# Performance work log

Hardware: AMD Instinct MI355X
Metric: run time of the kernel (lower is better)

Reference implementation:

```python
import jax, jax.numpy as jnp
import numpy as np

# NF4 quantization levels (16 entries) from NF4Quantizer
NF4_LEVELS = jnp.array([
    -1.0, -0.6961928009986877, -0.5250730514526367, -0.39491748809814453,
    -0.28444138169288635, -0.18477343022823334, -0.09105003625154495, 0.0,
    0.07958029955625534, 0.16093020141124725, 0.24611230194568634,
    0.33791524171829224, 0.44070982933044434, 0.5626170039176941,
    0.7229568362236023, 1.0], dtype=jnp.float32)

OUT_F, IN_F = 4096, 4096
B, S = 2, 512

def setup_inputs() -> dict:
    key = jax.random.key(0)
    k1, k2, k3, k4, k5 = jax.random.split(key, 5)
    x = jax.random.normal(k1, (B, S, IN_F), dtype=jnp.float32)
    w0 = jax.random.normal(k2, (OUT_F, IN_F), dtype=jnp.float32) * 0.02
    nf4_idx = jax.random.randint(k3, (OUT_F, IN_F), 0, 16, dtype=jnp.int32)
    scale = jax.random.uniform(k4, (1,), dtype=jnp.float32) * 0.1 + 0.01
    zero_point = jax.random.normal(k5, (1,), dtype=jnp.float32) * 0.01
    return {"x": x, "w0": w0, "nf4_idx": nf4_idx, "scale": scale,
            "zero_point": zero_point}

def reference(x, w0, nf4_idx, scale, zero_point):
    # NF4 dequantize: look up level values, then affine (quantized*scale + zp)
    q = NF4_LEVELS[nf4_idx]                      # [out, in] float32
    deq_w = q * scale + zero_point               # dequantized adaptor weight
    # frozen base linear + dequantized low-rank-adaptor linear (QLoRA-style)
    base = jnp.einsum('bsi,oi->bso', x, w0)
    adapt = jnp.einsum('bsi,oi->bso', x, deq_w)
    return base + adapt
```

## Files before the change

### kernel.cpp

```cpp
#include <hip/hip_runtime.h>
#include <hip/hip_bf16.h>
#include <stdint.h>

#define MDIM 1024
#define NDIM 4096
#define KDIM 4096

#define BM 128
#define BN 128
#define BK 64

typedef __attribute__((ext_vector_type(4))) float f32x4;
typedef __attribute__((ext_vector_type(4))) float float4v;
typedef __attribute__((ext_vector_type(4))) int int4v;
typedef __attribute__((ext_vector_type(4))) unsigned int uint4v;
typedef __attribute__((ext_vector_type(8))) short short8;

#define GLOBAL_AS __attribute__((address_space(1)))
#define LDS_AS __attribute__((address_space(3)))

#define HARD_BARRIER() do {                               \
    __builtin_amdgcn_sched_barrier(0);                    \
    asm volatile("s_waitcnt lgkmcnt(0)" ::: "memory");    \
    __builtin_amdgcn_s_barrier();                         \
    asm volatile("" ::: "memory");                        \
    __builtin_amdgcn_sched_barrier(0);                    \
} while (0)

__device__ __constant__ float c_nf4[16] = {
    -1.0f, -0.6961928009986877f, -0.5250730514526367f, -0.39491748809814453f,
    -0.28444138169288635f, -0.18477343022823334f, -0.09105003625154495f, 0.0f,
    0.07958029955625534f, 0.16093020141124725f, 0.24611230194568634f,
    0.33791524171829224f, 0.44070982933044434f, 0.5626170039176941f,
    0.7229568362236023f, 1.0f};

__device__ __forceinline__ unsigned bf16_rne(float f) {
    unsigned u = __float_as_uint(f);
    return (u + 0x7fffu + ((u >> 16) & 1u)) >> 16;
}

#define W_BLOCKS ((NDIM * KDIM) / (256 * 8))
#define X_BLOCKS ((MDIM * KDIM) / (256 * 8))

__global__ __launch_bounds__(256) void prep_kernel(
    const float* __restrict__ x, const float* __restrict__ w0,
    const int* __restrict__ nf4_idx, const float* __restrict__ scale_p,
    const float* __restrict__ zp_p, __hip_bfloat16* __restrict__ Wc,
    __hip_bfloat16* __restrict__ xb)
{
    const int lane = threadIdx.x & 63;
    if (blockIdx.x < W_BLOCKS) {
        const float scale = scale_p[0];
        const float zp = zp_p[0];
        const int tab = __float_as_int(c_nf4[lane & 15] * scale + zp);
        const size_t base = ((size_t)blockIdx.x * 256 + threadIdx.x) * 8;
        int4v i0 = *(const int4v*)(nf4_idx + base);
        int4v i1 = *(const int4v*)(nf4_idx + base + 4);
        float4v w_0 = *(const float4v*)(w0 + base);
        float4v w_1 = *(const float4v*)(w0 + base + 4);
        unsigned r[8];
#pragma unroll
        for (int j = 0; j < 4; j++) {
            float q = __int_as_float(__builtin_amdgcn_ds_bpermute(i0[j] * 4, tab));
            r[j] = bf16_rne(w_0[j] + q);
        }
#pragma unroll
        for (int j = 0; j < 4; j++) {
            float q = __int_as_float(__builtin_amdgcn_ds_bpermute(i1[j] * 4, tab));
            r[4 + j] = bf16_rne(w_1[j] + q);
        }
        uint4v st;
        st.x = r[0] | (r[1] << 16);
        st.y = r[2] | (r[3] << 16);
        st.z = r[4] | (r[5] << 16);
        st.w = r[6] | (r[7] << 16);
        *(uint4v*)((unsigned short*)Wc + base) = st;
    } else {
        const size_t base = ((size_t)(blockIdx.x - W_BLOCKS) * 256 + threadIdx.x) * 8;
        float4v a0 = *(const float4v*)(x + base);
        float4v a1 = *(const float4v*)(x + base + 4);
        uint4v st;
        st.x = bf16_rne(a0[0]) | (bf16_rne(a0[1]) << 16);
        st.y = bf16_rne(a0[2]) | (bf16_rne(a0[3]) << 16);
        st.z = bf16_rne(a1[0]) | (bf16_rne(a1[1]) << 16);
        st.w = bf16_rne(a1[2]) | (bf16_rne(a1[3]) << 16);
        *(uint4v*)((unsigned short*)xb + base) = st;
    }
}

__global__ __launch_bounds__(512) void gemm_kernel(
    const __hip_bfloat16* __restrict__ A,
    const __hip_bfloat16* __restrict__ B,
    float* __restrict__ C)
{
    __shared__ __hip_bfloat16 sm[3][2][BM * BK];

    const int tid = threadIdx.x;
    const int lane = tid & 63;
    const int w = tid >> 6;
    const int wr = w >> 2;
    const int wc = (w >> 1) & 1;
    const int wk = w & 1;

    const int bid = blockIdx.x;
    const int orig = (bid & 7) * 32 + (bid >> 3);
    const int mtile = orig & 7;
    const int ntile = orig >> 3;

    const int s_subrow = lane >> 3;
    const int s_chunkpos = lane & 7;
    int s_row[2], s_goff[2];
#pragma unroll
    for (int j = 0; j < 2; j++) {
        int row = w * 16 + j * 8 + s_subrow;
        s_row[j] = row;
        s_goff[j] = (s_chunkpos ^ (row & 7)) * 8;
    }

#define STAGE(buf, kt) do {                                                        \
    _Pragma("unroll")                                                              \
    for (int j = 0; j < 2; j++) {                                                  \
        const __hip_bfloat16* ga = A + (size_t)(mtile * BM + s_row[j]) * KDIM      \
                                     + (kt) * BK + s_goff[j];                      \
        __builtin_amdgcn_global_load_lds((const GLOBAL_AS void*)ga,                \
            (LDS_AS void*)&sm[buf][0][(w * 16 + j * 8) * BK], 16, 0, 0);           \
        const __hip_bfloat16* gb = B + (size_t)(ntile * BN + s_row[j]) * KDIM      \
                                     + (kt) * BK + s_goff[j];                      \
        __builtin_amdgcn_global_load_lds((const GLOBAL_AS void*)gb,                \
            (LDS_AS void*)&sm[buf][1][(w * 16 + j * 8) * BK], 16, 0, 0);           \
    }                                                                              \
} while (0)

    int a_off[4], b_off[4];
#pragma unroll
    for (int m = 0; m < 4; m++) {
        int row = wr * 64 + m * 16 + (lane & 15);
        int c = wk * 4 + (lane >> 4);
        a_off[m] = row * BK + (c ^ (row & 7)) * 8;
    }
#pragma unroll
    for (int n = 0; n < 4; n++) {
        int row = wc * 64 + n * 16 + (lane & 15);
        int c = wk * 4 + (lane >> 4);
        b_off[n] = row * BK + (c ^ (row & 7)) * 8;
    }

    f32x4 acc[4][4] = {};

#define COMPUTE(buf) do {                                                          \
    short8 af[4], bfv[4];                                                          \
    _Pragma("unroll")                                                              \
    for (int m = 0; m < 4; m++)                                                    \
        af[m] = *(const short8*)&sm[buf][0][a_off[m]];                             \
    _Pragma("unroll")                                                              \
    for (int n = 0; n < 4; n++)                                                    \
        bfv[n] = *(const short8*)&sm[buf][1][b_off[n]];                            \
    _Pragma("unroll")                                                              \
    for (int m = 0; m < 4; m++)                                                    \
        _Pragma("unroll")                                                          \
        for (int n = 0; n < 4; n++)                                                \
            acc[m][n] = __builtin_amdgcn_mfma_f32_16x16x32_bf16(                   \
                af[m], bfv[n], acc[m][n], 0, 0, 0);                                \
} while (0)

    const int NT = KDIM / BK;
    STAGE(0, 0);
    STAGE(1, 1);

    for (int t = 0; t < NT; t++) {
        const int cur = t % 3;
        if (t + 2 < NT) {
            STAGE((t + 2) % 3, t + 2);
            asm volatile("s_waitcnt vmcnt(8)" ::: "memory");
        } else if (t + 1 < NT) {
            asm volatile("s_waitcnt vmcnt(4)" ::: "memory");
        } else {
            asm volatile("s_waitcnt vmcnt(0)" ::: "memory");
        }
        HARD_BARRIER();
        COMPUTE(cur);
        HARD_BARRIER();
    }

    float* red = (float*)&sm[0][0][0];
    const int pair = wr * 2 + wc;
    if (wk == 1) {
#pragma unroll
        for (int m = 0; m < 4; m++) {
#pragma unroll
            for (int n = 0; n < 4; n++) {
                *(f32x4*)&red[pair * 4096 + (m * 4 + n) * 256 + lane * 4] =
                    acc[m][n];
            }
        }
    }
    HARD_BARRIER();
    if (wk == 0) {
        const int rbase = mtile * BM + wr * 64 + ((lane >> 4) << 2);
        const int cbase = ntile * BN + wc * 64 + (lane & 15);
#pragma unroll
        for (int m = 0; m < 4; m++) {
#pragma unroll
            for (int n = 0; n < 4; n++) {
                f32x4 other =
                    *(const f32x4*)&red[pair * 4096 + (m * 4 + n) * 256 + lane * 4];
                f32x4 v = acc[m][n] + other;
#pragma unroll
                for (int r = 0; r < 4; r++) {
                    C[(size_t)(rbase + m * 16 + r) * NDIM + cbase + n * 16] = v[r];
                }
            }
        }
    }
#undef STAGE
#undef COMPUTE
}

__global__ void fallback_kernel(const float* __restrict__ x,
                                const float* __restrict__ w0,
                                const int* __restrict__ nf4_idx,
                                const float* __restrict__ sp,
                                const float* __restrict__ zpp,
                                float* __restrict__ out)
{
    __shared__ float As[16][16], Bs[16][17];
    const int tx = threadIdx.x, ty = threadIdx.y;
    const int n0 = blockIdx.x * 16, m0 = blockIdx.y * 16;
    const float s = sp[0], zp = zpp[0];
    float acc = 0.0f;
    for (int k0 = 0; k0 < KDIM; k0 += 16) {
        As[ty][tx] = x[(size_t)(m0 + ty) * KDIM + k0 + tx];
        int id = nf4_idx[(size_t)(n0 + ty) * KDIM + k0 + tx];
        Bs[ty][tx] = w0[(size_t)(n0 + ty) * KDIM + k0 + tx] + c_nf4[id] * s + zp;
        __syncthreads();
#pragma unroll
        for (int j = 0; j < 16; j++) acc += As[ty][j] * Bs[tx][j];
        __syncthreads();
    }
    out[(size_t)(m0 + ty) * NDIM + n0 + tx] = acc;
}

extern "C" void kernel_launch(void* const* d_in, const int* in_sizes, int n_in,
                              void* d_out, int out_size, void* d_ws, size_t ws_size,
                              hipStream_t stream) {
    const float* x = (const float*)d_in[0];
    const float* w0 = (const float*)d_in[1];
    const int* nf4_idx = (const int*)d_in[2];
    const float* scale = (const float*)d_in[3];
    const float* zp = (const float*)d_in[4];
    float* out = (float*)d_out;

    const size_t wc_bytes = (size_t)NDIM * KDIM * 2;
    const size_t xb_bytes = (size_t)MDIM * KDIM * 2;

    if (ws_size >= wc_bytes + xb_bytes) {
        __hip_bfloat16* Wc = (__hip_bfloat16*)d_ws;
        __hip_bfloat16* xb = (__hip_bfloat16*)((char*)d_ws + wc_bytes);
        prep_kernel<<<W_BLOCKS + X_BLOCKS, 256, 0, stream>>>(
            x, w0, nf4_idx, scale, zp, Wc, xb);
        gemm_kernel<<<(MDIM / BM) * (NDIM / BN), 512, 0, stream>>>(xb, Wc, out);
    } else {
        fallback_kernel<<<dim3(NDIM / 16, MDIM / 16), dim3(16, 16), 0, stream>>>(
            x, w0, nf4_idx, scale, zp, out);
    }
}
```

Before: 74.38 us.

## Shrink GEMM tile to 128x64 with 256 threads and two blocks per CU

Halves the N tile of the bf16 GEMM to 64 and drops the block to 4 waves (2 row waves x 2 K-split waves), which doubles the grid to 512 blocks. Launch bounds now request 2 blocks per CU. The staging loads, LDS buffers, wait counts and split-K reduction are reworked to fit the new shape. The aim is to fill all 256 CUs with more blocks and raise occupancy, at the cost of lower operand reuse per block and more global traffic for A.

```diff
diff --git a/kernel.cpp b/kernel.cpp
--- a/kernel.cpp
+++ b/kernel.cpp
@@ -7,7 +7,7 @@
 #define KDIM 4096
 
 #define BM 128
-#define BN 128
+#define BN 64
 #define BK 64
 
 typedef __attribute__((ext_vector_type(4))) float f32x4;
@@ -88,46 +88,55 @@
     }
 }
 
-__global__ __launch_bounds__(512) void gemm_kernel(
+__global__ __launch_bounds__(256, 2) void gemm_kernel(
     const __hip_bfloat16* __restrict__ A,
     const __hip_bfloat16* __restrict__ B,
     float* __restrict__ C)
 {
-    __shared__ __hip_bfloat16 sm[3][2][BM * BK];
+    __shared__ __hip_bfloat16 smA[3][BM * BK];
+    __shared__ __hip_bfloat16 smB[3][BN * BK];
 
     const int tid = threadIdx.x;
     const int lane = tid & 63;
     const int w = tid >> 6;
-    const int wr = w >> 2;
-    const int wc = (w >> 1) & 1;
+    const int wr = w >> 1;
     const int wk = w & 1;
 
     const int bid = blockIdx.x;
-    const int orig = (bid & 7) * 32 + (bid >> 3);
+    const int orig = (bid & 7) * 64 + (bid >> 3);
     const int mtile = orig & 7;
     const int ntile = orig >> 3;
 
     const int s_subrow = lane >> 3;
     const int s_chunkpos = lane & 7;
-    int s_row[2], s_goff[2];
+    int a_row[4], a_goff[4], b_row[2], b_goff[2];
+#pragma unroll
+    for (int j = 0; j < 4; j++) {
+        int row = w * 32 + j * 8 + s_subrow;
+        a_row[j] = row;
+        a_goff[j] = (s_chunkpos ^ (row & 7)) * 8;
+    }
 #pragma unroll
     for (int j = 0; j < 2; j++) {
         int row = w * 16 + j * 8 + s_subrow;
-        s_row[j] = row;
-        s_goff[j] = (s_chunkpos ^ (row & 7)) * 8;
+        b_row[j] = row;
+        b_goff[j] = (s_chunkpos ^ (row & 7)) * 8;
     }
 
 #define STAGE(buf, kt) do {                                                        \
     _Pragma("unroll")                                                              \
+    for (int j = 0; j < 4; j++) {                                                  \
+        const __hip_bfloat16* ga = A + (size_t)(mtile * BM + a_row[j]) * KDIM      \
+                                     + (kt) * BK + a_goff[j];                      \
+        __builtin_amdgcn_global_load_lds((const GLOBAL_AS void*)ga,                \
+            (LDS_AS void*)&smA[buf][(w * 32 + j * 8) * BK], 16, 0, 0);             \
+    }                                                                              \
+    _Pragma("unroll")                                                              \
     for (int j = 0; j < 2; j++) {                                                  \
-        const __hip_bfloat16* ga = A + (size_t)(mtile * BM + s_row[j]) * KDIM      \
-                                     + (kt) * BK + s_goff[j];                      \
-        __builtin_amdgcn_global_load_lds((const GLOBAL_AS void*)ga,                \
-            (LDS_AS void*)&sm[buf][0][(w * 16 + j * 8) * BK], 16, 0, 0);           \
-        const __hip_bfloat16* gb = B + (size_t)(ntile * BN + s_row[j]) * KDIM      \
-                                     + (kt) * BK + s_goff[j];                      \
+        const __hip_bfloat16* gb = B + (size_t)(ntile * BN + b_row[j]) * KDIM      \
+                                     + (kt) * BK + b_goff[j];                      \
         __builtin_amdgcn_global_load_lds((const GLOBAL_AS void*)gb,                \
-            (LDS_AS void*)&sm[buf][1][(w * 16 + j * 8) * BK], 16, 0, 0);           \
+            (LDS_AS void*)&smB[buf][(w * 16 + j * 8) * BK], 16, 0, 0);             \
     }                                                                              \
 } while (0)
 
@@ -140,7 +149,7 @@
     }
 #pragma unroll
     for (int n = 0; n < 4; n++) {
-        int row = wc * 64 + n * 16 + (lane & 15);
+        int row = n * 16 + (lane & 15);
         int c = wk * 4 + (lane >> 4);
         b_off[n] = row * BK + (c ^ (row & 7)) * 8;
     }
@@ -151,10 +160,10 @@
     short8 af[4], bfv[4];                                                          \
     _Pragma("unroll")                                                              \
     for (int m = 0; m < 4; m++)                                                    \
-        af[m] = *(const short8*)&sm[buf][0][a_off[m]];                             \
+        af[m] = *(const short8*)&smA[buf][a_off[m]];                               \
     _Pragma("unroll")                                                              \
     for (int n = 0; n < 4; n++)                                                    \
-        bfv[n] = *(const short8*)&sm[buf][1][b_off[n]];                            \
+        bfv[n] = *(const short8*)&smB[buf][b_off[n]];                              \
     _Pragma("unroll")                                                              \
     for (int m = 0; m < 4; m++)                                                    \
         _Pragma("unroll")                                                          \
@@ -171,9 +180,9 @@
         const int cur = t % 3;
         if (t + 2 < NT) {
             STAGE((t + 2) % 3, t + 2);
-            asm volatile("s_waitcnt vmcnt(8)" ::: "memory");
+            asm volatile("s_waitcnt vmcnt(12)" ::: "memory");
         } else if (t + 1 < NT) {
-            asm volatile("s_waitcnt vmcnt(4)" ::: "memory");
+            asm volatile("s_waitcnt vmcnt(6)" ::: "memory");
         } else {
             asm volatile("s_waitcnt vmcnt(0)" ::: "memory");
         }
@@ -182,8 +191,8 @@
         HARD_BARRIER();
     }
 
-    float* red = (float*)&sm[0][0][0];
-    const int pair = wr * 2 + wc;
+    float* red = (float*)&smA[0][0];
+    const int pair = wr;
     if (wk == 1) {
 #pragma unroll
         for (int m = 0; m < 4; m++) {
@@ -197,7 +206,7 @@
     HARD_BARRIER();
     if (wk == 0) {
         const int rbase = mtile * BM + wr * 64 + ((lane >> 4) << 2);
-        const int cbase = ntile * BN + wc * 64 + (lane & 15);
+        const int cbase = ntile * BN + (lane & 15);
 #pragma unroll
         for (int m = 0; m < 4; m++) {
 #pragma unroll
@@ -258,7 +267,7 @@
         __hip_bfloat16* xb = (__hip_bfloat16*)((char*)d_ws + wc_bytes);
         prep_kernel<<<W_BLOCKS + X_BLOCKS, 256, 0, stream>>>(
             x, w0, nf4_idx, scale, zp, Wc, xb);
-        gemm_kernel<<<(MDIM / BM) * (NDIM / BN), 512, 0, stream>>>(xb, Wc, out);
+        gemm_kernel<<<(MDIM / BM) * (NDIM / BN), 256, 0, stream>>>(xb, Wc, out);
     } else {
         fallback_kernel<<<dim3(NDIM / 16, MDIM / 16), dim3(16, 16), 0, stream>>>(
             x, w0, nf4_idx, scale, zp, out);
```

Result: slower. 83.47 us (+12.2%).
